# Optimization experiments

Measured on AMD Instinct MI355X. Metric: run time of the kernel, lower is better.

## Reference

```python
import jax, jax.numpy as jnp
import numpy as np

B, NC, H, GH = 64, 21, 32, 64  # batch, num_class, hidden spatial, geo spatial
DN = ('NCHW', 'OIHW', 'NCHW')


def conv2d(x, w, b, stride, pad):
    y = jax.lax.conv_general_dilated(x, w, (stride, stride), [(pad, pad), (pad, pad)], dimension_numbers=DN)
    return y + b[None, :, None, None]


def group_norm(x, scale, bias, groups=32, eps=1e-5):
    b, c, h, w = x.shape
    xg = x.reshape(b, groups, c // groups, h, w)
    mean = xg.mean(axis=(2, 3, 4), keepdims=True)
    var = xg.var(axis=(2, 3, 4), keepdims=True)
    xn = ((xg - mean) * jax.lax.rsqrt(var + eps)).reshape(b, c, h, w)
    return xn * scale[None, :, None, None] + bias[None, :, None, None]


def setup_inputs() -> dict:
    key = jax.random.key(0)
    ks = iter(jax.random.split(key, 64))
    rn = lambda shape, s=0.05: jax.random.normal(next(ks), shape, jnp.float32) * s
    inp = {
        'hidden_state': jnp.tanh(rn((B, 128, H, H), 1.0)),
        'delta_flow': rn((B, 2, H, H), 1.0),
        'mask': jax.random.uniform(next(ks), (B, 1, H, H), jnp.float32),
        'geo': rn((B, 8, GH, GH), 1.0),
        'obj_id': jax.random.randint(next(ks), (B,), 1, NC + 1),
        # geo_model
        'g1_w': rn((128, 8, 3, 3)), 'g1_b': rn((128,)),
        'g2_w': rn((64, 128, 3, 3)), 'g2_b': rn((64,)),
        # delta_flow_model
        'd1_w': rn((128, 2, 7, 7)), 'd1_b': rn((128,)),
        'd2_w': rn((64, 128, 3, 3)), 'd2_b': rn((64,)),
        # mask_model
        'm1_w': rn((64, 1, 3, 3)), 'm1_b': rn((64,)),
        'm2_w': rn((32, 64, 3, 3)), 'm2_b': rn((32,)),
        # conv_layers (conv + GroupNorm(32) x3, all stride 2)
        'c1_w': rn((128, 288, 3, 3)), 'c1_b': rn((128,)), 'gn1_s': jnp.ones((128,)), 'gn1_bb': jnp.zeros((128,)),
        'c2_w': rn((128, 128, 3, 3)), 'c2_b': rn((128,)), 'gn2_s': jnp.ones((128,)), 'gn2_bb': jnp.zeros((128,)),
        'c3_w': rn((128, 128, 3, 3)), 'c3_b': rn((128,)), 'gn3_s': jnp.ones((128,)), 'gn3_bb': jnp.zeros((128,)),
        # fc_layers
        'fc1_w': rn((1024, 2048)), 'fc1_b': rn((1024,)),
        'fc2_w': rn((256, 1024)), 'fc2_b': rn((256,)),
        # prediction heads (random instead of zero-init so grads are non-trivial)
        'rot_w': rn((6 * NC, 256)), 'rot_b': jnp.tile(jnp.array([1., 0., 0., 0., 1., 0.], jnp.float32), NC),
        'tr_w': rn((3 * NC, 256)), 'tr_b': rn((3 * NC,)),
    }
    return inp


def reference(hidden_state, delta_flow, mask, geo, obj_id,
              g1_w, g1_b, g2_w, g2_b, d1_w, d1_b, d2_w, d2_b, m1_w, m1_b, m2_w, m2_b,
              c1_w, c1_b, gn1_s, gn1_bb, c2_w, c2_b, gn2_s, gn2_bb, c3_w, c3_b, gn3_s, gn3_bb,
              fc1_w, fc1_b, fc2_w, fc2_b, rot_w, rot_b, tr_w, tr_b):
    relu = jax.nn.relu
    geo_enc = relu(conv2d(relu(conv2d(geo, g1_w, g1_b, 1, 1)), g2_w, g2_b, 2, 1))        # [B,64,32,32]
    df_enc = relu(conv2d(relu(conv2d(delta_flow, d1_w, d1_b, 1, 3)), d2_w, d2_b, 1, 1))  # [B,64,32,32]
    m_enc = relu(conv2d(relu(conv2d(mask, m1_w, m1_b, 1, 1)), m2_w, m2_b, 1, 1))         # [B,32,32,32]
    enc = jnp.concatenate([hidden_state, df_enc, m_enc, geo_enc], axis=1)                # [B,288,32,32]
    x = relu(group_norm(conv2d(enc, c1_w, c1_b, 2, 1), gn1_s, gn1_bb))                   # [B,128,16,16]
    x = relu(group_norm(conv2d(x, c2_w, c2_b, 2, 1), gn2_s, gn2_bb))                     # [B,128,8,8]
    x = relu(group_norm(conv2d(x, c3_w, c3_b, 2, 1), gn3_s, gn3_bb))                     # [B,128,4,4]
    x = x.reshape(x.shape[0], -1)                                                        # [B,2048]
    x = relu(x @ fc1_w.T + fc1_b)
    x = relu(x @ fc2_w.T + fc2_b)                                                        # [B,256]
    tr = (x @ tr_w.T + tr_b).reshape(-1, NC, 3)
    rot = (x @ rot_w.T + rot_b).reshape(-1, NC, 6)
    # torch.index_select(., dim=1, index=obj_id-1)[:, 0, :] -> uses obj_id[0]
    tr = jnp.take(tr, obj_id - 1, axis=1)[:, 0, :]
    rot = jnp.take(rot, obj_id - 1, axis=1)[:, 0, :]
    return (rot, tr)
```

## Files before the change

### kernel.cpp

```cpp
#include <hip/hip_runtime.h>
#include <hip/hip_bf16.h>

typedef __bf16 bf16x8 __attribute__((ext_vector_type(8)));
typedef __bf16 bf16x4 __attribute__((ext_vector_type(4)));
typedef float  f32x4  __attribute__((ext_vector_type(4)));

struct PackArgs {
    const float* src[11];
    __bf16* dst[11];
    int Cout[11], Cin[11], KHW[11], KW[11], Cinpad[11], Kpad[11], mode[11];
    int cum[12];
};

__device__ void pack_dev(const PackArgs& pa, int gidx)
{
    if (gidx >= pa.cum[11]) return;
    int s = 0;
    for (int i = 1; i <= 10; ++i) s += (gidx >= pa.cum[i]) ? 1 : 0;
    int l = gidx - pa.cum[s];
    int Kp = pa.Kpad[s];
    int co = l / Kp, k = l - co * Kp;
    float v = 0.f;
    if (co < pa.Cout[s]) {
        if (pa.mode[s] == 0) {
            int cip = pa.Cinpad[s];
            int tap = k / cip, ci = k - tap * cip;
            if (tap < pa.KHW[s] && ci < pa.Cin[s])
                v = pa.src[s][((long)co * pa.Cin[s] + ci) * pa.KHW[s] + tap];
        } else if (pa.mode[s] == 1) {
            int pix = k >> 7, c = k & 127;
            v = pa.src[s][(long)co * 2048 + c * 16 + pix];
        } else if (pa.mode[s] == 2) {
            v = pa.src[s][(long)co * Kp + k];
        } else {
            int kh = k >> 4, r = k & 15, kw = r >> 1, ci = r & 1;
            if (kh < 7 && kw < 7)
                v = pa.src[s][((long)(co * 2 + ci) * 7 + kh) * 7 + kw];
        }
    }
    pa.dst[s][l] = (__bf16)v;
}

struct BulkPack { const float* s[8]; __bf16* d[8]; };

template<int CO, int CIN, int KP>
__device__ __forceinline__ void pack_conv8(const float* __restrict__ src,
                                           __bf16* __restrict__ dst, int eb)
{
    int e = eb * 8;
    int co = e / KP;
    int k  = e - co * KP;
    int tap = k / CIN;
    int ci  = k - tap * CIN;
    bf16x8 o = {};
    if (co < CO && tap < 9) {
        const float* s = src + ((long)co * CIN + ci) * 9 + tap;
#pragma unroll
        for (int j = 0; j < 8; ++j) o[j] = (__bf16)s[j * 9];
    }
    *(bf16x8*)&dst[e] = o;
}

__device__ __forceinline__ void pack_fc1_8(const float* __restrict__ src,
                                           __bf16* __restrict__ dst, int eb)
{
    int e = eb * 8;
    int co = e >> 11, k = e & 2047;
    int pix = k >> 7, c = k & 127;
    const float* s = src + (long)co * 2048 + c * 16 + pix;
    bf16x8 o;
#pragma unroll
    for (int j = 0; j < 8; ++j) o[j] = (__bf16)s[j * 16];
    *(bf16x8*)&dst[e] = o;
}

__device__ __forceinline__ void pack_fc2_8(const float* __restrict__ src,
                                           __bf16* __restrict__ dst, int eb)
{
    int e = eb * 8;
    f32x4 lo = *(const f32x4*)&src[e];
    f32x4 hi = *(const f32x4*)&src[e + 4];
    bf16x8 o = { (__bf16)lo.x, (__bf16)lo.y, (__bf16)lo.z, (__bf16)lo.w,
                 (__bf16)hi.x, (__bf16)hi.y, (__bf16)hi.z, (__bf16)hi.w };
    *(bf16x8*)&dst[e] = o;
// ... 245 lines not shown
    bf16x8 av[APASS], bv[BPASS];
    auto LOAD = [&](int k0) {
        int k = k0 + scol;
#pragma unroll
        for (int ja = 0; ja < APASS; ++ja)
            av[ja] = *(const bf16x8*)&A[(long)(ja * SROWS + srow) * g.Kpad + k];
        if (MODE == 1) {
            int q = k >> 3;
            int off = (q >> 1) * (g.Win * g.CinTot) + (q & 1) * 8;
#pragma unroll
            for (int j = 0; j < BPASS; ++j)
                bv[j] = *(const bf16x8*)&in_[nbase[j] + off];
        } else {
            int tap = k / CINPAD;
            int ci  = k - tap * CINPAD;
            int kh  = tap / KW;
            int kw  = tap - kh * KW;
            bool tv = tap < g.KHW;
            int off = (kh * g.Win + kw) * g.CinTot + ci;
#pragma unroll
            for (int j = 0; j < BPASS; ++j) {
                bf16x8 z = {};
                int hi = hi0a[j] + kh, wi = wi0a[j] + kw;
                if (tv && (unsigned)hi < (unsigned)g.Hin && (unsigned)wi < (unsigned)g.Win)
                    z = *(const bf16x8*)&in_[nbase[j] + off];
                bv[j] = z;
            }
        }
    };

    f32x4 acc[MFRAG][2] = {};
    LOAD(0);
    for (int k0 = 0;;) {
        if (k0) __syncthreads();
#pragma unroll
        for (int ja = 0; ja < APASS; ++ja)
            *(bf16x8*)&As[ja * SROWS + srow][scol] = av[ja];
#pragma unroll
        for (int j = 0; j < BPASS; ++j)
            *(bf16x8*)&Bs[j * SROWS + srow][scol] = bv[j];
        __syncthreads();
        int kn = k0 + BK;
        bool more = kn < g.Kpad;
        if (more) LOAD(kn);
#pragma unroll
        for (int kk = 0; kk < BK; kk += 32) {
            bf16x8 bfr[2];
            bfr[0] = *(const bf16x8*)&Bs[wn + lr][kk + lk];
            bfr[1] = *(const bf16x8*)&Bs[wn + 16 + lr][kk + lk];
#pragma unroll
            for (int i = 0; i < MFRAG; ++i) {
                bf16x8 a = *(const bf16x8*)&As[wm + i * 16 + lr][kk + lk];
                acc[i][0] = __builtin_amdgcn_mfma_f32_16x16x32_bf16(a, bfr[0], acc[i][0], 0, 0, 0);
                acc[i][1] = __builtin_amdgcn_mfma_f32_16x16x32_bf16(a, bfr[1], acc[i][1], 0, 0, 0);
            }
        }
        if (!more) break;
        k0 = kn;
    }

    const int HWm1 = (1 << g.log2HWout) - 1;
#pragma unroll
    for (int i = 0; i < MFRAG; ++i) {
        int co = wm + i * 16 + (lane >> 4) * 4;
        if (co >= g.Cout) continue;
        f32x4 bv4 = *(const f32x4*)&bias[co];
#pragma unroll
        for (int jb = 0; jb < 2; ++jb) {
            int nn = ntile + wn + jb * 16 + lr;
            f32x4 v = acc[i][jb] + bv4;
            if (RELU) { v.x = fmaxf(v.x, 0.f); v.y = fmaxf(v.y, 0.f); v.z = fmaxf(v.z, 0.f); v.w = fmaxf(v.w, 0.f); }
            int ob = nn >> g.log2HWout, opix = nn & HWm1;
            long o = (((long)(g.b0o + ob) << g.log2HWout) + opix) * g.CTOT + g.C0 + co;
            if (OUTBF) {
                bf16x4 o4 = { (__bf16)v.x, (__bf16)v.y, (__bf16)v.z, (__bf16)v.w };
                *(bf16x4*)&((__bf16*)out_)[o] = o4;
            } else {
                *(f32x4*)&((float*)out_)[o] = v;
            }
        }
    }
}

template<int BM, int BN, int BK, int THREADS, int WMW, int WNW, int CINPAD, int KW, int MODE, bool OUTBF, bool RELU>
__global__ __launch_bounds__(THREADS) void conv_gemm2(
    const __bf16* __restrict__ in_, const __bf16* __restrict__ A,
    const float* __restrict__ bias, void* __restrict__ out_, ConvGeom g)
{
    __shared__ __attribute__((aligned(16))) char smem[(BM + BN) * (BK + 8) * 2];
    int mt = blockIdx.y * BM;
    ConvGeom gg = g;
    gg.C0 += mt;
    gg.Cout -= mt;
    conv_dev2<BM, BN, BK, THREADS, WMW, WNW, CINPAD, KW, MODE, OUTBF, RELU>(
        smem, blockIdx.x, in_, A + (long)mt * g.Kpad, bias + mt, out_, gg);
}

template<int BM, int BN, int BK, int THREADS, int WMW, int WNW, int CINPAD, int KW, int PPB>
__global__ __launch_bounds__(THREADS) void conv_gn_kern(
    const __bf16* __restrict__ in_, const __bf16* __restrict__ A,
    const float* __restrict__ bias, const float* __restrict__ gns,
    const float* __restrict__ gnb, __bf16* __restrict__ out_, ConvGeom g)
{
    constexpr int MEXT = BM / WMW;
    constexpr int NEXT = BN / WNW;
    constexpr int MFRAG = MEXT / 16;
    constexpr int NFRAG = NEXT / 16;
    constexpr int KROW = BK / 8;
    constexpr int SROWS = THREADS / KROW;
    constexpr int APASS = BM / SROWS;
    constexpr int BPASS = BN / SROWS;
    constexpr int LDK = BK + 8;

    __shared__ __attribute__((aligned(16))) char smem_[(BM + BN) * (BK + 8) * 2];
    auto As = reinterpret_cast<__bf16 (*)[LDK]>(smem_);
    auto Bs = reinterpret_cast<__bf16 (*)[LDK]>(smem_ + (size_t)BM * LDK * sizeof(__bf16));
    static_assert((size_t)BN * (BM + 4) * 4 <= (size_t)(BM + BN) * (BK + 8) * 2, "smf fits");

    const int tid = threadIdx.x;
    const int mt = blockIdx.y * BM;
    const __bf16* Ap = A + (long)mt * g.Kpad;
    const int C0 = g.C0 + mt;
    const int ntile = blockIdx.x * BN;
    const int lane = tid & 63, w = tid >> 6;
    const int wm = (w / WNW) * MEXT, wn = (w % WNW) * NEXT;
    const int lr = lane & 15, lk = (lane >> 4) * 8;
    const int srow = tid / KROW, scol = (tid % KROW) * 8;

    long nbase[BPASS]; int hi0a[BPASS], wi0a[BPASS];
#pragma unroll
    for (int j = 0; j < BPASS; ++j) {
        int n = ntile + j * SROWS + srow;
        int bb = g.b0i + (n >> g.log2HWout);
        int pix = n & ((1 << g.log2HWout) - 1);
        int ho = pix >> g.log2Wout, wo = pix & ((1 << g.log2Wout) - 1);
        hi0a[j] = ho * g.stride - g.pad;
        wi0a[j] = wo * g.stride - g.pad;
        nbase[j] = (((long)bb * g.Hin + hi0a[j]) * g.Win + wi0a[j]) * g.CinTot;
    }

    bf16x8 av[APASS], bv[BPASS];
    auto LOAD = [&](int k0) {
        int k = k0 + scol;
#pragma unroll
        for (int ja = 0; ja < APASS; ++ja)
            av[ja] = *(const bf16x8*)&Ap[(long)(ja * SROWS + srow) * g.Kpad + k];
        int tap = k / CINPAD;
        int ci  = k - tap * CINPAD;
        int kh  = tap / KW;
        int kw  = tap - kh * KW;
        bool tv = tap < g.KHW;
        int off = (kh * g.Win + kw) * g.CinTot + ci;
#pragma unroll
        for (int j = 0; j < BPASS; ++j) {
            bf16x8 z = {};
            int hi = hi0a[j] + kh, wi = wi0a[j] + kw;
            if (tv && (unsigned)hi < (unsigned)g.Hin && (unsigned)wi < (unsigned)g.Win)
                z = *(const bf16x8*)&in_[nbase[j] + off];
            bv[j] = z;
        }
    };

    f32x4 acc[MFRAG][NFRAG] = {};
    LOAD(0);
    for (int k0 = 0;;) {
        if (k0) __syncthreads();
#pragma unroll
        for (int ja = 0; ja < APASS; ++ja)
            *(bf16x8*)&As[ja * SROWS + srow][scol] = av[ja];
#pragma unroll
        for (int j = 0; j < BPASS; ++j)
            *(bf16x8*)&Bs[j * SROWS + srow][scol] = bv[j];
        __syncthreads();
        int kn = k0 + BK;
        bool more = kn < g.Kpad;
        if (more) LOAD(kn);
#pragma unroll
        for (int kk = 0; kk < BK; kk += 32) {
            bf16x8 bfr[NFRAG], afr[MFRAG];
#pragma unroll
            for (int jn = 0; jn < NFRAG; ++jn)
                bfr[jn] = *(const bf16x8*)&Bs[wn + jn * 16 + lr][kk + lk];
#pragma unroll
            for (int i = 0; i < MFRAG; ++i)
                afr[i] = *(const bf16x8*)&As[wm + i * 16 + lr][kk + lk];
#pragma unroll
            for (int i = 0; i < MFRAG; ++i)
#pragma unroll
                for (int jn = 0; jn < NFRAG; ++jn)
                    acc[i][jn] = __builtin_amdgcn_mfma_f32_16x16x32_bf16(afr[i], bfr[jn], acc[i][jn], 0, 0, 0);
        }
        if (!more) break;
        k0 = kn;
    }

    __syncthreads();
    auto smf = reinterpret_cast<float (*)[BM + 4]>(smem_);
#pragma unroll
    for (int i = 0; i < MFRAG; ++i) {
        int m = wm + i * 16 + (lane >> 4) * 4;
        f32x4 bv4 = *(const f32x4*)&bias[C0 + m];
#pragma unroll
        for (int jn = 0; jn < NFRAG; ++jn) {
            int n = wn + jn * 16 + lr;
            *(f32x4*)&smf[n][m] = acc[i][jn] + bv4;
        }
    }
    __syncthreads();

    constexpr int NSETS = (BN / PPB) * (BM / 4);
    constexpr int TPS = THREADS / NSETS;
    constexpr int PPT = PPB / TPS;
    const int set = tid / TPS, part = tid % TPS;
    const int bit = set / (BM / 4);
    const int grp = set % (BM / 4);
    const int m0 = grp * 4;
    float sum = 0.f, sq = 0.f;
#pragma unroll
    for (int p = 0; p < PPT; ++p) {
        int nl = bit * PPB + part + p * TPS;
        f32x4 v = *(const f32x4*)&smf[nl][m0];
        sum += v.x + v.y + v.z + v.w;
        sq  += v.x * v.x + v.y * v.y + v.z * v.z + v.w * v.w;
    }
#pragma unroll
    for (int off = TPS >> 1; off > 0; off >>= 1) {
        sum += __shfl_xor(sum, off);
        sq  += __shfl_xor(sq, off);
    }
    const float len = (float)(PPB * 4);
    float mean = sum / len;
    float var  = sq / len - mean * mean;
    float rstd = rsqrtf(fmaxf(var, 0.f) + 1e-5f);
    f32x4 s4 = *(const f32x4*)&gns[C0 + m0];
    f32x4 b4 = *(const f32x4*)&gnb[C0 + m0];
    const int HWm1 = (1 << g.log2HWout) - 1;
#pragma unroll
    for (int p = 0; p < PPT; ++p) {
        int nl = bit * PPB + part + p * TPS;
        f32x4 v = *(const f32x4*)&smf[nl][m0];
        f32x4 r;
        r.x = fmaxf((v.x - mean) * rstd * s4.x + b4.x, 0.f);
        r.y = fmaxf((v.y - mean) * rstd * s4.y + b4.y, 0.f);
        r.z = fmaxf((v.z - mean) * rstd * s4.z + b4.z, 0.f);
        r.w = fmaxf((v.w - mean) * rstd * s4.w + b4.w, 0.f);
        int n = ntile + nl;
        int ob = n >> g.log2HWout, opix = n & HWm1;
        long o = (((long)(g.b0o + ob) << g.log2HWout) + opix) * g.CTOT + C0 + m0;
        bf16x4 o4 = { (__bf16)r.x, (__bf16)r.y, (__bf16)r.z, (__bf16)r.w };
        *(bf16x4*)&out_[o] = o4;
    }
}

#define B1_CONV 3072
#define B1_PACK 775
__global__ __launch_bounds__(512) void branch1_kern(
    const __bf16* __restrict__ geo_p, const __bf16* __restrict__ wg1, const float* __restrict__ g1_b, __bf16* __restrict__ g1out,
    const __bf16* __restrict__ dflow_pp, const __bf16* __restrict__ wd1, const float* __restrict__ d1_b, __bf16* __restrict__ d1out,
    const __bf16* __restrict__ mask_p, const __bf16* __restrict__ wm1, const float* __restrict__ m1_b, __bf16* __restrict__ m1out,
    BulkPack bp, ConvGeom gg1, ConvGeom gd1, ConvGeom gm1)
{
    __shared__ __attribute__((aligned(16))) char smem[27648];
    int x = blockIdx.x;
    if (x < 2048) {
        conv_dev<128, 128, 32, 512, 8, 3, 0, true, true>(smem, x, geo_p, wg1, g1_b, g1out, gg1);
        return;
    }
    if (x < 2560) {
        conv_dev<128, 128, 32, 512, 8, 7, 1, true, true>(smem, x - 2048, dflow_pp, wd1, d1_b, d1out, gd1);
        return;
    }
    if (x < B1_CONV) {
        conv_dev<64, 128, 64, 512, 8, 3, 0, true, true>(smem, x - 2560, mask_p, wm1, m1_b, m1out, gm1);
        return;
    }
    int x2 = x - B1_CONV;
    int tid = threadIdx.x;
    if (x2 < 18)       pack_conv8<64, 128, 1152>(bp.s[0], bp.d[0], x2 * 512 + tid);
    else if (x2 < 36)  pack_conv8<64, 128, 1152>(bp.s[1], bp.d[1], (x2 - 18) * 512 + tid);
    else if (x2 < 45)  pack_conv8<32, 64, 576>(bp.s[2], bp.d[2], (x2 - 36) * 512 + tid);
    else if (x2 < 127) pack_conv8<128, 288, 2624>(bp.s[3], bp.d[3], (x2 - 45) * 512 + tid);
    else if (x2 < 163) pack_conv8<128, 128, 1152>(bp.s[4], bp.d[4], (x2 - 127) * 512 + tid);
    else if (x2 < 199) pack_conv8<128, 128, 1152>(bp.s[5], bp.d[5], (x2 - 163) * 512 + tid);
    else if (x2 < 711) pack_fc1_8(bp.s[6], bp.d[6], (x2 - 199) * 512 + tid);
    else               pack_fc2_8(bp.s[7], bp.d[7], (x2 - 711) * 512 + tid);
}

#define B2_CONV 1536
#define B2_HID 4096
__global__ __launch_bounds__(256) void branch2_kern(
    const __bf16* __restrict__ g1out, const __bf16* __restrict__ wg2, const float* __restrict__ g2_b,
    const __bf16* __restrict__ d1out, const __bf16* __restrict__ wd2, const float* __restrict__ d2_b,
    const __bf16* __restrict__ m1out, const __bf16* __restrict__ wm2, const float* __restrict__ m2_b,
    const float* __restrict__ hidden, __bf16* __restrict__ enc,
    ConvGeom gg2, ConvGeom gd2, ConvGeom gm2)
{
    __shared__ __attribute__((aligned(16))) char smem[(64 + 128) * (64 + 8) * 2];
    int x = blockIdx.x;
    if (x >= B2_CONV) { hid_dev(smem, hidden, enc, x - B2_CONV, threadIdx.x); return; }
    int sec = x % 3, bx = x / 3;
    if (sec == 0)
        conv_dev2<64, 128, 64, 256, 1, 4, 128, 3, 0, true, true>(smem, bx, g1out, wg2, g2_b, enc, gg2);
    else if (sec == 1)
        conv_dev2<64, 128, 64, 256, 1, 4, 128, 3, 0, true, true>(smem, bx, d1out, wd2, d2_b, enc, gd2);
    else
        conv_dev2<64, 128, 64, 256, 1, 4, 64, 3, 0, true, true>(smem, bx, m1out, wm2, m2_b, enc, gm2);
}

__global__ __launch_bounds__(256) void fc1_splitk(
    const __bf16* __restrict__ A, const __bf16* __restrict__ B,
    float* __restrict__ outacc)
{
    __shared__ __attribute__((aligned(16))) __bf16 As[64][40];
    __shared__ __attribute__((aligned(16))) __bf16 Bs[64][40];
    const int tid = threadIdx.x;
    const int mtile = blockIdx.y * 64;
    const int kbase = blockIdx.x * 512;
    const int lane = tid & 63, w = tid >> 6;
    const int wm = (w >> 1) * 32, wn = (w & 1) * 32;
    const int lr = lane & 15, lk = (lane >> 4) * 8;
    const int srow = tid >> 2, soff = (tid & 3) * 8;

    f32x4 acc00 = {}, acc01 = {}, acc10 = {}, acc11 = {};
    for (int k0 = 0; k0 < 512; k0 += 32) {
        *(bf16x8*)&As[srow][soff] = *(const bf16x8*)&A[(long)(mtile + srow) * 2048 + kbase + k0 + soff];
        *(bf16x8*)&Bs[srow][soff] = *(const bf16x8*)&B[(long)srow * 2048 + kbase + k0 + soff];
        __syncthreads();
        bf16x8 a0 = *(const bf16x8*)&As[wm + lr][lk];
        bf16x8 a1 = *(const bf16x8*)&As[wm + 16 + lr][lk];
        bf16x8 b0f = *(const bf16x8*)&Bs[wn + lr][lk];
        bf16x8 b1f = *(const bf16x8*)&Bs[wn + 16 + lr][lk];
        acc00 = __builtin_amdgcn_mfma_f32_16x16x32_bf16(a0, b0f, acc00, 0, 0, 0);
        acc01 = __builtin_amdgcn_mfma_f32_16x16x32_bf16(a0, b1f, acc01, 0, 0, 0);
        acc10 = __builtin_amdgcn_mfma_f32_16x16x32_bf16(a1, b0f, acc10, 0, 0, 0);
        acc11 = __builtin_amdgcn_mfma_f32_16x16x32_bf16(a1, b1f, acc11, 0, 0, 0);
        __syncthreads();
    }
    f32x4 accs[2][2] = { { acc00, acc01 }, { acc10, acc11 } };
#pragma unroll
    for (int mi = 0; mi < 2; ++mi) {
        int co0 = mtile + wm + mi * 16 + (lane >> 4) * 4;
#pragma unroll
        for (int ni = 0; ni < 2; ++ni) {
            int nn = wn + ni * 16 + lr;
            f32x4 v = accs[mi][ni];
            float* dst = &outacc[(long)nn * 1024 + co0];
            atomicAdd(dst + 0, v.x);
            atomicAdd(dst + 1, v.y);
            atomicAdd(dst + 2, v.z);
            atomicAdd(dst + 3, v.w);
        }
    }
}

__global__ __launch_bounds__(256) void fc2_splitk(
    const __bf16* __restrict__ A, const float* __restrict__ Bacc,
    const float* __restrict__ bb, float* __restrict__ outacc)
{
    __shared__ __attribute__((aligned(16))) __bf16 As[64][40];
    __shared__ __attribute__((aligned(16))) __bf16 Bs[64][40];
    const int tid = threadIdx.x;
    const int mtile = blockIdx.y * 64;
    const int kbase = blockIdx.x * 256;
    const int lane = tid & 63, w = tid >> 6;
    const int wm = (w >> 1) * 32, wn = (w & 1) * 32;
    const int lr = lane & 15, lk = (lane >> 4) * 8;
    const int srow = tid >> 2, soff = (tid & 3) * 8;

    f32x4 acc00 = {}, acc01 = {}, acc10 = {}, acc11 = {};
    for (int k0 = 0; k0 < 256; k0 += 32) {
        int k = kbase + k0 + soff;
        *(bf16x8*)&As[srow][soff] = *(const bf16x8*)&A[(long)(mtile + srow) * 1024 + k];
        f32x4 lo = *(const f32x4*)&Bacc[(long)srow * 1024 + k];
        f32x4 hi = *(const f32x4*)&Bacc[(long)srow * 1024 + k + 4];
        f32x4 blo = *(const f32x4*)&bb[k];
        f32x4 bhi = *(const f32x4*)&bb[k + 4];
        bf16x8 bvv;
        bvv[0] = (__bf16)fmaxf(lo.x + blo.x, 0.f);
        bvv[1] = (__bf16)fmaxf(lo.y + blo.y, 0.f);
        bvv[2] = (__bf16)fmaxf(lo.z + blo.z, 0.f);
        bvv[3] = (__bf16)fmaxf(lo.w + blo.w, 0.f);
        bvv[4] = (__bf16)fmaxf(hi.x + bhi.x, 0.f);
        bvv[5] = (__bf16)fmaxf(hi.y + bhi.y, 0.f);
        bvv[6] = (__bf16)fmaxf(hi.z + bhi.z, 0.f);
        bvv[7] = (__bf16)fmaxf(hi.w + bhi.w, 0.f);
        *(bf16x8*)&Bs[srow][soff] = bvv;
        __syncthreads();
        bf16x8 a0 = *(const bf16x8*)&As[wm + lr][lk];
        bf16x8 a1 = *(const bf16x8*)&As[wm + 16 + lr][lk];
        bf16x8 b0f = *(const bf16x8*)&Bs[wn + lr][lk];
        bf16x8 b1f = *(const bf16x8*)&Bs[wn + 16 + lr][lk];
        acc00 = __builtin_amdgcn_mfma_f32_16x16x32_bf16(a0, b0f, acc00, 0, 0, 0);
        acc01 = __builtin_amdgcn_mfma_f32_16x16x32_bf16(a0, b1f, acc01, 0, 0, 0);
        acc10 = __builtin_amdgcn_mfma_f32_16x16x32_bf16(a1, b0f, acc10, 0, 0, 0);
        acc11 = __builtin_amdgcn_mfma_f32_16x16x32_bf16(a1, b1f, acc11, 0, 0, 0);
        __syncthreads();
    }
    f32x4 accs[2][2] = { { acc00, acc01 }, { acc10, acc11 } };
#pragma unroll
    for (int mi = 0; mi < 2; ++mi) {
        int co0 = mtile + wm + mi * 16 + (lane >> 4) * 4;
#pragma unroll
        for (int ni = 0; ni < 2; ++ni) {
            int nn = wn + ni * 16 + lr;
            f32x4 v = accs[mi][ni];
            float* dst = &outacc[(long)nn * 256 + co0];
            atomicAdd(dst + 0, v.x);
            atomicAdd(dst + 1, v.y);
            atomicAdd(dst + 2, v.z);
            atomicAdd(dst + 3, v.w);
        }
    }
}

__global__ void gn_nhwc(const float* __restrict__ in, const float* __restrict__ s,
                        const float* __restrict__ bi, __bf16* __restrict__ out,
                        int C, int HW)
{
    int b = blockIdx.x >> 5, g = blockIdx.x & 31;
    int tid = threadIdx.x, nt = blockDim.x;
    const float* p = in + (long)b * HW * C + g * 4;
    float sum = 0.f, sq = 0.f;
    for (int i = tid; i < HW; i += nt) {
        f32x4 v = *(const f32x4*)&p[(long)i * C];
        sum += v.x + v.y + v.z + v.w;
        sq  += v.x * v.x + v.y * v.y + v.z * v.z + v.w * v.w;
    }
    __shared__ float rs[256], rq[256];
    rs[tid] = sum; rq[tid] = sq; __syncthreads();
    for (int off = nt >> 1; off > 0; off >>= 1) {
        if (tid < off) { rs[tid] += rs[tid + off]; rq[tid] += rq[tid + off]; }
        __syncthreads();
    }
    int len = HW * 4;
    float mean = rs[0] / len;
    float var  = rq[0] / len - mean * mean;
    float rstd = rsqrtf(fmaxf(var, 0.f) + 1e-5f);
    f32x4 s4 = *(const f32x4*)&s[g * 4];
    f32x4 b4 = *(const f32x4*)&bi[g * 4];
    __bf16* q = out + (long)b * HW * C + g * 4;
    for (int i = tid; i < HW; i += nt) {
        f32x4 v = *(const f32x4*)&p[(long)i * C];
        f32x4 r;
        r.x = fmaxf((v.x - mean) * rstd * s4.x + b4.x, 0.f);
        r.y = fmaxf((v.y - mean) * rstd * s4.y + b4.y, 0.f);
        r.z = fmaxf((v.z - mean) * rstd * s4.z + b4.z, 0.f);
        r.w = fmaxf((v.w - mean) * rstd * s4.w + b4.w, 0.f);
        bf16x4 o4 = { (__bf16)r.x, (__bf16)r.y, (__bf16)r.z, (__bf16)r.w };
        *(bf16x4*)&q[(long)i * C] = o4;
    }
}

__global__ __launch_bounds__(576) void head_kern(
    const float* __restrict__ x, const float* __restrict__ fb,
    const float* __restrict__ rw, const float* __restrict__ rb,
    const float* __restrict__ tw, const float* __restrict__ tb,
    const int* __restrict__ obj, float* __restrict__ out)
{
    int b = blockIdx.x;
    int k = threadIdx.x >> 6;
    int lane = threadIdx.x & 63;
    int j = obj[0] - 1;
    const float* xr = x + (long)b * 256;
    const float* wr;
    float bias0;
    if (k < 6) { wr = rw + (long)(j * 6 + k) * 256; bias0 = rb[j * 6 + k]; }
    else       { wr = tw + (long)(j * 3 + (k - 6)) * 256; bias0 = tb[j * 3 + (k - 6)]; }
    float acc = 0.f;
#pragma unroll
    for (int p = 0; p < 4; ++p) {
        int i = lane + p * 64;
        float xv = fmaxf(xr[i] + fb[i], 0.f);
        acc = fmaf(xv, wr[i], acc);
    }
#pragma unroll
    for (int off = 32; off > 0; off >>= 1) acc += __shfl_down(acc, off);
    if (lane == 0) {
        float r = acc + bias0;
        if (k < 6) out[b * 6 + k] = r;
        else       out[384 + b * 3 + (k - 6)] = r;
    }
}

extern "C" void kernel_launch(void* const* d_in, const int* in_sizes, int n_in,
                              void* d_out, int out_size, void* d_ws, size_t ws_size,
                              hipStream_t stream)
{
    const float* hidden = (const float*)d_in[0];
    const float* dflow  = (const float*)d_in[1];
    const float* mask   = (const float*)d_in[2];
    const float* geo    = (const float*)d_in[3];
    const int*   obj    = (const int*)d_in[4];
    const float* g1_w = (const float*)d_in[5],  *g1_b = (const float*)d_in[6];
    const float* g2_w = (const float*)d_in[7],  *g2_b = (const float*)d_in[8];
    const float* d1_w = (const float*)d_in[9],  *d1_b = (const float*)d_in[10];
    const float* d2_w = (const float*)d_in[11], *d2_b = (const float*)d_in[12];
    const float* m1_w = (const float*)d_in[13], *m1_b = (const float*)d_in[14];
    const float* m2_w = (const float*)d_in[15], *m2_b = (const float*)d_in[16];
    const float* c1_w = (const float*)d_in[17], *c1_b = (const float*)d_in[18];
    const float* gn1_s = (const float*)d_in[19], *gn1_bb = (const float*)d_in[20];
    const float* c2_w = (const float*)d_in[21], *c2_b = (const float*)d_in[22];
    const float* gn2_s = (const float*)d_in[23], *gn2_bb = (const float*)d_in[24];
    const float* c3_w = (const float*)d_in[25], *c3_b = (const float*)d_in[26];
    const float* gn3_s = (const float*)d_in[27], *gn3_bb = (const float*)d_in[28];
    const float* fc1_w = (const float*)d_in[29], *fc1_b = (const float*)d_in[30];
    const float* fc2_w = (const float*)d_in[31], *fc2_b = (const float*)d_in[32];
    const float* rot_w = (const float*)d_in[33], *rot_b = (const float*)d_in[34];
    const float* tr_w  = (const float*)d_in[35], *tr_b  = (const float*)d_in[36];

    char* ws = (char*)d_ws;
    __bf16* enc = (__bf16*)ws;
    char* W = ws + 37748736;
    __bf16* wg1  = (__bf16*)(W + 0);
    __bf16* wd1  = (__bf16*)(W + 24576);
    __bf16* wm1  = (__bf16*)(W + 57344);
    __bf16* wg2  = (__bf16*)(W + 73728);
    __bf16* wd2  = (__bf16*)(W + 221184);
    __bf16* wm2  = (__bf16*)(W + 368640);
    __bf16* wc1  = (__bf16*)(W + 442368);
    __bf16* wc2  = (__bf16*)(W + 1114112);
    __bf16* wc3  = (__bf16*)(W + 1409024);
    __bf16* wfc1 = (__bf16*)(W + 1703936);
    __bf16* wfc2 = (__bf16*)(W + 5898240);
    __bf16* geo_p    = (__bf16*)(ws + 44179456);
    __bf16* dflow_pp = (__bf16*)(ws + 48373760);
    __bf16* mask_p   = (__bf16*)(ws + 48783360);
    __bf16* g1out    = (__bf16*)(ws + 49831936);
    __bf16* d1out    = (__bf16*)(ws + 116940800);
    __bf16* m1out    = (__bf16*)(ws + 133718016);
    float*  c1raw    = (float*)(ws + 142106624);
    __bf16* x1       = (__bf16*)(ws + 150495232);
    __bf16* x2       = (__bf16*)(ws + 156786688);
    __bf16* x3       = (__bf16*)(ws + 158359552);
    float*  fc1acc   = (float*)(ws + 158621696);
    float*  fc2acc   = (float*)(ws + 158883840);

    PackArgs pa;
    {
        const float* srcs[11] = { g1_w, d1_w, m1_w, g2_w, d2_w, m2_w, c1_w, c2_w, c3_w, fc1_w, fc2_w };
        __bf16* dsts[11] = { wg1, wd1, wm1, wg2, wd2, wm2, wc1, wc2, wc3, wfc1, wfc2 };
        int Co[11]  = { 128, 128, 64, 64, 64, 32, 128, 128, 128, 1024, 256 };
        int Ci[11]  = { 8, 2, 1, 128, 128, 64, 288, 128, 128, 0, 0 };
        int KH[11]  = { 9, 49, 9, 9, 9, 9, 9, 9, 9, 0, 0 };
        int KWn[11] = { 3, 7, 3, 3, 3, 3, 3, 3, 3, 0, 0 };
        int Cp[11]  = { 8, 8, 8, 128, 128, 64, 288, 128, 128, 0, 0 };
        int Kp[11]  = { 96, 128, 128, 1152, 1152, 576, 2624, 1152, 1152, 2048, 1024 };
        int Mp[11]  = { 128, 128, 64, 64, 64, 64, 128, 128, 128, 1024, 256 };
        int Md[11]  = { 0, 3, 0, 0, 0, 0, 0, 0, 0, 1, 2 };
        int c = 0; pa.cum[0] = 0;
        for (int i = 0; i < 11; ++i) {
            pa.src[i] = srcs[i]; pa.dst[i] = dsts[i];
            pa.Cout[i] = Co[i]; pa.Cin[i] = Ci[i]; pa.KHW[i] = KH[i]; pa.KW[i] = KWn[i];
            pa.Cinpad[i] = Cp[i]; pa.Kpad[i] = Kp[i]; pa.mode[i] = Md[i];
            c += Mp[i] * Kp[i]; pa.cum[i + 1] = c;
        }
    }
    BulkPack bp;
    {
        const float* s[8] = { g2_w, d2_w, m2_w, c1_w, c2_w, c3_w, fc1_w, fc2_w };
        __bf16* d[8] = { wg2, wd2, wm2, wc1, wc2, wc3, wfc1, wfc2 };
        for (int i = 0; i < 8; ++i) { bp.s[i] = s[i]; bp.d[i] = d[i]; }
    }

    {
        int total_blocks = PACK_B + GEOV_B + DF_B + MASKV_B + ZERO_B;
        prep_kern<<<dim3(total_blocks), 256, 0, stream>>>(pa, geo, geo_p, dflow, dflow_pp,
                                                          mask, mask_p, fc1acc, fc2acc);
    }

    {
        ConvGeom gg1 = { 8, 64, 64, 12, 6, 1, 1, 96, 9, 128, 128, 0, 0, 0 };
        ConvGeom gd1 = { 2, 40, 40, 10, 5, 1, 0, 128, 49, 128, 128, 0, 0, 0 };
        ConvGeom gm1 = { 8, 32, 32, 10, 5, 1, 1, 128, 9, 64, 64, 0, 0, 0 };
        branch1_kern<<<dim3(B1_CONV + B1_PACK), 512, 0, stream>>>(geo_p, wg1, g1_b, g1out,
                                                                  dflow_pp, wd1, d1_b, d1out,
                                                                  mask_p, wm1, m1_b, m1out,
                                                                  bp, gg1, gd1, gm1);
    }
    {
        ConvGeom gg2 = { 128, 64, 64, 10, 5, 2, 1, 1152, 9, 64, 288, 224, 0, 0 };
        ConvGeom gd2 = { 128, 32, 32, 10, 5, 1, 1, 1152, 9, 64, 288, 128, 0, 0 };
        ConvGeom gm2 = { 64, 32, 32, 10, 5, 1, 1, 576, 9, 32, 288, 192, 0, 0 };
        branch2_kern<<<dim3(B2_CONV + B2_HID), 256, 0, stream>>>(g1out, wg2, g2_b,
                                                                 d1out, wd2, d2_b,
                                                                 m1out, wm2, m2_b,
                                                                 hidden, enc, gg2, gd2, gm2);
    }

    {
        ConvGeom gc1 = { 288, 32, 32, 8, 4, 2, 1, 2624, 9, 128, 128, 0, 0, 0 };
        conv_gemm2<64, 128, 64, 256, 1, 4, 288, 3, 0, false, false><<<dim3(128, 2), 256, 0, stream>>>(enc, wc1, c1_b, c1raw, gc1);
    }
    gn_nhwc<<<dim3(2048), 256, 0, stream>>>(c1raw, gn1_s, gn1_bb, x1, 128, 256);

    {
        ConvGeom gc2 = { 128, 16, 16, 6, 3, 2, 1, 1152, 9, 128, 128, 0, 0, 0 };
        conv_gn_kern<64, 64, 64, 256, 2, 2, 128, 3, 64><<<dim3(64, 2), 256, 0, stream>>>(
            x1, wc2, c2_b, gn2_s, gn2_bb, x2, gc2);
    }
    {
        ConvGeom gc3 = { 128, 8, 8, 4, 2, 2, 1, 1152, 9, 128, 128, 0, 0, 0 };
        conv_gn_kern<64, 64, 64, 256, 2, 2, 128, 3, 16><<<dim3(16, 2), 256, 0, stream>>>(
            x2, wc3, c3_b, gn3_s, gn3_bb, x3, gc3);
    }

    fc1_splitk<<<dim3(4, 16), 256, 0, stream>>>(wfc1, x3, fc1acc);
    fc2_splitk<<<dim3(4, 4), 256, 0, stream>>>(wfc2, fc1acc, fc1_b, fc2acc);

    head_kern<<<dim3(64), 576, 0, stream>>>(fc2acc, fc2_b, rot_w, rot_b, tr_w, tr_b, obj, (float*)d_out);
}
```

Baseline: 205.5 us.

## Fuse tail stages into one cooperative kernel with grid-wide syncs

Replaces the seven tail launches (conv1, group norm, conv2+GN, conv3+GN, fc1, fc2, head) with a single cooperative kernel of 256 blocks. Each stage runs on a subset of blocks and the stages are separated by grid.sync(). The goal is to remove per-launch overhead and the idle gaps between many small dependent kernels. In exchange, grid barriers have their own cost, later stages leave most blocks idle, and the head now runs with 256 threads looping over the outputs.

```diff
diff --git a/kernel.cpp b/kernel.cpp
--- a/kernel.cpp
+++ b/kernel.cpp
@@ -1,5 +1,8 @@
 #include <hip/hip_runtime.h>
 #include <hip/hip_bf16.h>
+#include <hip/hip_cooperative_groups.h>
+
+namespace cg = cooperative_groups;
 
 typedef __bf16 bf16x8 __attribute__((ext_vector_type(8)));
 typedef __bf16 bf16x4 __attribute__((ext_vector_type(4)));
@@ -411,25 +414,11 @@
     }
 }
 
-template<int BM, int BN, int BK, int THREADS, int WMW, int WNW, int CINPAD, int KW, int MODE, bool OUTBF, bool RELU>
-__global__ __launch_bounds__(THREADS) void conv_gemm2(
-    const __bf16* __restrict__ in_, const __bf16* __restrict__ A,
-    const float* __restrict__ bias, void* __restrict__ out_, ConvGeom g)
-{
-    __shared__ __attribute__((aligned(16))) char smem[(BM + BN) * (BK + 8) * 2];
-    int mt = blockIdx.y * BM;
-    ConvGeom gg = g;
-    gg.C0 += mt;
-    gg.Cout -= mt;
-    conv_dev2<BM, BN, BK, THREADS, WMW, WNW, CINPAD, KW, MODE, OUTBF, RELU>(
-        smem, blockIdx.x, in_, A + (long)mt * g.Kpad, bias + mt, out_, gg);
-}
-
 template<int BM, int BN, int BK, int THREADS, int WMW, int WNW, int CINPAD, int KW, int PPB>
-__global__ __launch_bounds__(THREADS) void conv_gn_kern(
+__device__ void conv_gn_dev(char* __restrict__ smem_, int bx, int my,
     const __bf16* __restrict__ in_, const __bf16* __restrict__ A,
     const float* __restrict__ bias, const float* __restrict__ gns,
-    const float* __restrict__ gnb, __bf16* __restrict__ out_, ConvGeom g)
+    const float* __restrict__ gnb, __bf16* __restrict__ out_, const ConvGeom& g)
 {
     constexpr int MEXT = BM / WMW;
     constexpr int NEXT = BN / WNW;
@@ -441,16 +430,14 @@
     constexpr int BPASS = BN / SROWS;
     constexpr int LDK = BK + 8;
 
-    __shared__ __attribute__((aligned(16))) char smem_[(BM + BN) * (BK + 8) * 2];
     auto As = reinterpret_cast<__bf16 (*)[LDK]>(smem_);
     auto Bs = reinterpret_cast<__bf16 (*)[LDK]>(smem_ + (size_t)BM * LDK * sizeof(__bf16));
-    static_assert((size_t)BN * (BM + 4) * 4 <= (size_t)(BM + BN) * (BK + 8) * 2, "smf fits");
 
     const int tid = threadIdx.x;
-    const int mt = blockIdx.y * BM;
+    const int mt = my * BM;
     const __bf16* Ap = A + (long)mt * g.Kpad;
     const int C0 = g.C0 + mt;
-    const int ntile = blockIdx.x * BN;
+    const int ntile = bx * BN;
     const int lane = tid & 63, w = tid >> 6;
     const int wm = (w / WNW) * MEXT, wn = (w % WNW) * NEXT;
     const int lr = lane & 15, lk = (lane >> 4) * 8;
@@ -579,72 +566,57 @@
         bf16x4 o4 = { (__bf16)r.x, (__bf16)r.y, (__bf16)r.z, (__bf16)r.w };
         *(bf16x4*)&out_[o] = o4;
     }
-}
-
-#define B1_CONV 3072
-#define B1_PACK 775
-__global__ __launch_bounds__(512) void branch1_kern(
-    const __bf16* __restrict__ geo_p, const __bf16* __restrict__ wg1, const float* __restrict__ g1_b, __bf16* __restrict__ g1out,
-    const __bf16* __restrict__ dflow_pp, const __bf16* __restrict__ wd1, const float* __restrict__ d1_b, __bf16* __restrict__ d1out,
-    const __bf16* __restrict__ mask_p, const __bf16* __restrict__ wm1, const float* __restrict__ m1_b, __bf16* __restrict__ m1out,
-    BulkPack bp, ConvGeom gg1, ConvGeom gd1, ConvGeom gm1)
-{
-    __shared__ __attribute__((aligned(16))) char smem[27648];
-    int x = blockIdx.x;
-    if (x < 2048) {
-        conv_dev<128, 128, 32, 512, 8, 3, 0, true, true>(smem, x, geo_p, wg1, g1_b, g1out, gg1);
-        return;
-    }
-    if (x < 2560) {
-        conv_dev<128, 128, 32, 512, 8, 7, 1, true, true>(smem, x - 2048, dflow_pp, wd1, d1_b, d1out, gd1);
-        return;
-    }
-    if (x < B1_CONV) {
-        conv_dev<64, 128, 64, 512, 8, 3, 0, true, true>(smem, x - 2560, mask_p, wm1, m1_b, m1out, gm1);
-        return;
-    }
-    int x2 = x - B1_CONV;
-    int tid = threadIdx.x;
-    if (x2 < 18)       pack_conv8<64, 128, 1152>(bp.s[0], bp.d[0], x2 * 512 + tid);
-    else if (x2 < 36)  pack_conv8<64, 128, 1152>(bp.s[1], bp.d[1], (x2 - 18) * 512 + tid);
-    else if (x2 < 45)  pack_conv8<32, 64, 576>(bp.s[2], bp.d[2], (x2 - 36) * 512 + tid);
-    else if (x2 < 127) pack_conv8<128, 288, 2624>(bp.s[3], bp.d[3], (x2 - 45) * 512 + tid);
-    else if (x2 < 163) pack_conv8<128, 128, 1152>(bp.s[4], bp.d[4], (x2 - 127) * 512 + tid);
-    else if (x2 < 199) pack_conv8<128, 128, 1152>(bp.s[5], bp.d[5], (x2 - 163) * 512 + tid);
-    else if (x2 < 711) pack_fc1_8(bp.s[6], bp.d[6], (x2 - 199) * 512 + tid);
-    else               pack_fc2_8(bp.s[7], bp.d[7], (x2 - 711) * 512 + tid);
-}
-
-#define B2_CONV 1536
-#define B2_HID 4096
-__global__ __launch_bounds__(256) void branch2_kern(
-    const __bf16* __restrict__ g1out, const __bf16* __restrict__ wg2, const float* __restrict__ g2_b,
-    const __bf16* __restrict__ d1out, const __bf16* __restrict__ wd2, const float* __restrict__ d2_b,
-    const __bf16* __restrict__ m1out, const __bf16* __restrict__ wm2, const float* __restrict__ m2_b,
-    const float* __restrict__ hidden, __bf16* __restrict__ enc,
-    ConvGeom gg2, ConvGeom gd2, ConvGeom gm2)
-{
-    __shared__ __attribute__((aligned(16))) char smem[(64 + 128) * (64 + 8) * 2];
-    int x = blockIdx.x;
-    if (x >= B2_CONV) { hid_dev(smem, hidden, enc, x - B2_CONV, threadIdx.x); return; }
-    int sec = x % 3, bx = x / 3;
-    if (sec == 0)
-        conv_dev2<64, 128, 64, 256, 1, 4, 128, 3, 0, true, true>(smem, bx, g1out, wg2, g2_b, enc, gg2);
-    else if (sec == 1)
-        conv_dev2<64, 128, 64, 256, 1, 4, 128, 3, 0, true, true>(smem, bx, d1out, wd2, d2_b, enc, gd2);
-    else
-        conv_dev2<64, 128, 64, 256, 1, 4, 64, 3, 0, true, true>(smem, bx, m1out, wm2, m2_b, enc, gm2);
-}
-
-__global__ __launch_bounds__(256) void fc1_splitk(
-    const __bf16* __restrict__ A, const __bf16* __restrict__ B,
-    float* __restrict__ outacc)
-{
-    __shared__ __attribute__((aligned(16))) __bf16 As[64][40];
-    __shared__ __attribute__((aligned(16))) __bf16 Bs[64][40];
+    __syncthreads();
+}
+
+__device__ void gn_dev(char* smem, const float* __restrict__ in, const float* __restrict__ s,
+                       const float* __restrict__ bi, __bf16* __restrict__ out,
+                       int C, int HW, int unit, int tid)
+{
+    int b = unit >> 5, g = unit & 31;
+    const float* p = in + (long)b * HW * C + g * 4;
+    float sum = 0.f, sq = 0.f;
+    for (int i = tid; i < HW; i += 256) {
+        f32x4 v = *(const f32x4*)&p[(long)i * C];
+        sum += v.x + v.y + v.z + v.w;
+        sq  += v.x * v.x + v.y * v.y + v.z * v.z + v.w * v.w;
+    }
+    float* rs = (float*)smem;
+    float* rq = rs + 256;
+    rs[tid] = sum; rq[tid] = sq; __syncthreads();
+    for (int off = 128; off > 0; off >>= 1) {
+        if (tid < off) { rs[tid] += rs[tid + off]; rq[tid] += rq[tid + off]; }
+        __syncthreads();
+    }
+    int len = HW * 4;
+    float mean = rs[0] / len;
+    float var  = rq[0] / len - mean * mean;
+    float rstd = rsqrtf(fmaxf(var, 0.f) + 1e-5f);
+    f32x4 s4 = *(const f32x4*)&s[g * 4];
+    f32x4 b4 = *(const f32x4*)&bi[g * 4];
+    __bf16* q = out + (long)b * HW * C + g * 4;
+    for (int i = tid; i < HW; i += 256) {
+        f32x4 v = *(const f32x4*)&p[(long)i * C];
+        f32x4 r;
+        r.x = fmaxf((v.x - mean) * rstd * s4.x + b4.x, 0.f);
+        r.y = fmaxf((v.y - mean) * rstd * s4.y + b4.y, 0.f);
+        r.z = fmaxf((v.z - mean) * rstd * s4.z + b4.z, 0.f);
+        r.w = fmaxf((v.w - mean) * rstd * s4.w + b4.w, 0.f);
+        bf16x4 o4 = { (__bf16)r.x, (__bf16)r.y, (__bf16)r.z, (__bf16)r.w };
+        *(bf16x4*)&q[(long)i * C] = o4;
+    }
+    __syncthreads();
+}
+
+__device__ void fc1_dev(char* smem, int kchunk, int mt,
+                        const __bf16* __restrict__ A, const __bf16* __restrict__ B,
+                        float* __restrict__ outacc)
+{
+    auto As = reinterpret_cast<__bf16 (*)[40]>(smem);
+    auto Bs = reinterpret_cast<__bf16 (*)[40]>(smem + 64 * 40 * 2);
     const int tid = threadIdx.x;
-    const int mtile = blockIdx.y * 64;
-    const int kbase = blockIdx.x * 512;
+    const int mtile = mt * 64;
+    const int kbase = kchunk * 512;
     const int lane = tid & 63, w = tid >> 6;
     const int wm = (w >> 1) * 32, wn = (w & 1) * 32;
     const int lr = lane & 15, lk = (lane >> 4) * 8;
@@ -682,15 +654,15 @@
     }
 }
 
-__global__ __launch_bounds__(256) void fc2_splitk(
-    const __bf16* __restrict__ A, const float* __restrict__ Bacc,
-    const float* __restrict__ bb, float* __restrict__ outacc)
-{
-    __shared__ __attribute__((aligned(16))) __bf16 As[64][40];
-    __shared__ __attribute__((aligned(16))) __bf16 Bs[64][40];
+__device__ void fc2_dev(char* smem, int kchunk, int mt,
+                        const __bf16* __restrict__ A, const float* __restrict__ Bacc,
+                        const float* __restrict__ bb, float* __restrict__ outacc)
+{
+    auto As = reinterpret_cast<__bf16 (*)[40]>(smem);
+    auto Bs = reinterpret_cast<__bf16 (*)[40]>(smem + 64 * 40 * 2);
     const int tid = threadIdx.x;
-    const int mtile = blockIdx.y * 64;
-    const int kbase = blockIdx.x * 256;
+    const int mtile = mt * 64;
+    const int kbase = kchunk * 256;
     const int lane = tid & 63, w = tid >> 6;
     const int wm = (w >> 1) * 32, wn = (w & 1) * 32;
     const int lr = lane & 15, lk = (lane >> 4) * 8;
@@ -742,73 +714,140 @@
     }
 }
 
-__global__ void gn_nhwc(const float* __restrict__ in, const float* __restrict__ s,
-                        const float* __restrict__ bi, __bf16* __restrict__ out,
-                        int C, int HW)
-{
-    int b = blockIdx.x >> 5, g = blockIdx.x & 31;
-    int tid = threadIdx.x, nt = blockDim.x;
-    const float* p = in + (long)b * HW * C + g * 4;
-    float sum = 0.f, sq = 0.f;
-    for (int i = tid; i < HW; i += nt) {
-        f32x4 v = *(const f32x4*)&p[(long)i * C];
-        sum += v.x + v.y + v.z + v.w;
-        sq  += v.x * v.x + v.y * v.y + v.z * v.z + v.w * v.w;
-    }
-    __shared__ float rs[256], rq[256];
-    rs[tid] = sum; rq[tid] = sq; __syncthreads();
-    for (int off = nt >> 1; off > 0; off >>= 1) {
-        if (tid < off) { rs[tid] += rs[tid + off]; rq[tid] += rq[tid + off]; }
-        __syncthreads();
-    }
-    int len = HW * 4;
-    float mean = rs[0] / len;
-    float var  = rq[0] / len - mean * mean;
-    float rstd = rsqrtf(fmaxf(var, 0.f) + 1e-5f);
-    f32x4 s4 = *(const f32x4*)&s[g * 4];
-    f32x4 b4 = *(const f32x4*)&bi[g * 4];
-    __bf16* q = out + (long)b * HW * C + g * 4;
-    for (int i = tid; i < HW; i += nt) {
-        f32x4 v = *(const f32x4*)&p[(long)i * C];
-        f32x4 r;
-        r.x = fmaxf((v.x - mean) * rstd * s4.x + b4.x, 0.f);
-        r.y = fmaxf((v.y - mean) * rstd * s4.y + b4.y, 0.f);
-        r.z = fmaxf((v.z - mean) * rstd * s4.z + b4.z, 0.f);
-        r.w = fmaxf((v.w - mean) * rstd * s4.w + b4.w, 0.f);
-        bf16x4 o4 = { (__bf16)r.x, (__bf16)r.y, (__bf16)r.z, (__bf16)r.w };
-        *(bf16x4*)&q[(long)i * C] = o4;
-    }
-}
-
-__global__ __launch_bounds__(576) void head_kern(
-    const float* __restrict__ x, const float* __restrict__ fb,
-    const float* __restrict__ rw, const float* __restrict__ rb,
-    const float* __restrict__ tw, const float* __restrict__ tb,
-    const int* __restrict__ obj, float* __restrict__ out)
-{
-    int b = blockIdx.x;
-    int k = threadIdx.x >> 6;
-    int lane = threadIdx.x & 63;
+__device__ void head_dev(const float* __restrict__ x, const float* __restrict__ fb,
+                         const float* __restrict__ rw, const float* __restrict__ rb,
+                         const float* __restrict__ tw, const float* __restrict__ tb,
+                         const int* __restrict__ obj, float* __restrict__ out,
+                         int b, int tid)
+{
+    int wid = tid >> 6, lane = tid & 63;
     int j = obj[0] - 1;
     const float* xr = x + (long)b * 256;
-    const float* wr;
-    float bias0;
-    if (k < 6) { wr = rw + (long)(j * 6 + k) * 256; bias0 = rb[j * 6 + k]; }
-    else       { wr = tw + (long)(j * 3 + (k - 6)) * 256; bias0 = tb[j * 3 + (k - 6)]; }
-    float acc = 0.f;
-#pragma unroll
-    for (int p = 0; p < 4; ++p) {
-        int i = lane + p * 64;
-        float xv = fmaxf(xr[i] + fb[i], 0.f);
-        acc = fmaf(xv, wr[i], acc);
-    }
-#pragma unroll
-    for (int off = 32; off > 0; off >>= 1) acc += __shfl_down(acc, off);
-    if (lane == 0) {
-        float r = acc + bias0;
-        if (k < 6) out[b * 6 + k] = r;
-        else       out[384 + b * 3 + (k - 6)] = r;
-    }
+    for (int k = wid; k < 9; k += 4) {
+        const float* wr;
+        float b0;
+        if (k < 6) { wr = rw + (long)(j * 6 + k) * 256; b0 = rb[j * 6 + k]; }
+        else       { wr = tw + (long)(j * 3 + (k - 6)) * 256; b0 = tb[j * 3 + (k - 6)]; }
+        float acc = 0.f;
+#pragma unroll
+        for (int p = 0; p < 4; ++p) {
+            int i = lane + p * 64;
+            float xv = fmaxf(xr[i] + fb[i], 0.f);
+            acc = fmaf(xv, wr[i], acc);
+        }
+#pragma unroll
+        for (int off = 32; off > 0; off >>= 1) acc += __shfl_down(acc, off);
+        if (lane == 0) {
+            float r = acc + b0;
+            if (k < 6) out[b * 6 + k] = r;
+            else       out[384 + b * 3 + (k - 6)] = r;
+        }
+    }
+}
+
+#define B1_CONV 3072
+#define B1_PACK 775
+__global__ __launch_bounds__(512) void branch1_kern(
+    const __bf16* __restrict__ geo_p, const __bf16* __restrict__ wg1, const float* __restrict__ g1_b, __bf16* __restrict__ g1out,
+    const __bf16* __restrict__ dflow_pp, const __bf16* __restrict__ wd1, const float* __restrict__ d1_b, __bf16* __restrict__ d1out,
+    const __bf16* __restrict__ mask_p, const __bf16* __restrict__ wm1, const float* __restrict__ m1_b, __bf16* __restrict__ m1out,
+    BulkPack bp, ConvGeom gg1, ConvGeom gd1, ConvGeom gm1)
+{
+    __shared__ __attribute__((aligned(16))) char smem[27648];
+    int x = blockIdx.x;
+    if (x < 2048) {
+        conv_dev<128, 128, 32, 512, 8, 3, 0, true, true>(smem, x, geo_p, wg1, g1_b, g1out, gg1);
+        return;
+    }
+    if (x < 2560) {
+        conv_dev<128, 128, 32, 512, 8, 7, 1, true, true>(smem, x - 2048, dflow_pp, wd1, d1_b, d1out, gd1);
+        return;
+    }
+    if (x < B1_CONV) {
+        conv_dev<64, 128, 64, 512, 8, 3, 0, true, true>(smem, x - 2560, mask_p, wm1, m1_b, m1out, gm1);
+        return;
+    }
+    int x2 = x - B1_CONV;
+    int tid = threadIdx.x;
+    if (x2 < 18)       pack_conv8<64, 128, 1152>(bp.s[0], bp.d[0], x2 * 512 + tid);
+    else if (x2 < 36)  pack_conv8<64, 128, 1152>(bp.s[1], bp.d[1], (x2 - 18) * 512 + tid);
+    else if (x2 < 45)  pack_conv8<32, 64, 576>(bp.s[2], bp.d[2], (x2 - 36) * 512 + tid);
+    else if (x2 < 127) pack_conv8<128, 288, 2624>(bp.s[3], bp.d[3], (x2 - 45) * 512 + tid);
+    else if (x2 < 163) pack_conv8<128, 128, 1152>(bp.s[4], bp.d[4], (x2 - 127) * 512 + tid);
+    else if (x2 < 199) pack_conv8<128, 128, 1152>(bp.s[5], bp.d[5], (x2 - 163) * 512 + tid);
+    else if (x2 < 711) pack_fc1_8(bp.s[6], bp.d[6], (x2 - 199) * 512 + tid);
+    else               pack_fc2_8(bp.s[7], bp.d[7], (x2 - 711) * 512 + tid);
+}
+
+#define B2_CONV 1536
+#define B2_HID 4096
+__global__ __launch_bounds__(256) void branch2_kern(
+    const __bf16* __restrict__ g1out, const __bf16* __restrict__ wg2, const float* __restrict__ g2_b,
+    const __bf16* __restrict__ d1out, const __bf16* __restrict__ wd2, const float* __restrict__ d2_b,
+    const __bf16* __restrict__ m1out, const __bf16* __restrict__ wm2, const float* __restrict__ m2_b,
+    const float* __restrict__ hidden, __bf16* __restrict__ enc,
+    ConvGeom gg2, ConvGeom gd2, ConvGeom gm2)
+{
+    __shared__ __attribute__((aligned(16))) char smem[(64 + 128) * (64 + 8) * 2];
+    int x = blockIdx.x;
+    if (x >= B2_CONV) { hid_dev(smem, hidden, enc, x - B2_CONV, threadIdx.x); return; }
+    int sec = x % 3, bx = x / 3;
+    if (sec == 0)
+        conv_dev2<64, 128, 64, 256, 1, 4, 128, 3, 0, true, true>(smem, bx, g1out, wg2, g2_b, enc, gg2);
+    else if (sec == 1)
+        conv_dev2<64, 128, 64, 256, 1, 4, 128, 3, 0, true, true>(smem, bx, d1out, wd2, d2_b, enc, gd2);
+    else
+        conv_dev2<64, 128, 64, 256, 1, 4, 64, 3, 0, true, true>(smem, bx, m1out, wm2, m2_b, enc, gm2);
+}
+
+struct TailArgs {
+    const __bf16 *enc, *wc1, *wc2, *wc3, *wfc1, *wfc2;
+    const float *c1_b, *gn1_s, *gn1_bb, *c2_b, *gn2_s, *gn2_bb, *c3_b, *gn3_s, *gn3_bb;
+    const float *fc1_b, *fc2_b, *rot_w, *rot_b, *tr_w, *tr_b;
+    const int* obj;
+    float* c1raw;
+    __bf16 *x1, *x2, *x3;
+    float *fc1acc, *fc2acc, *out;
+    ConvGeom gc1, gc2, gc3;
+};
+
+__global__ __launch_bounds__(256) void tail_kern(TailArgs a)
+{
+    __shared__ __attribute__((aligned(16))) char smem[27648];
+    cg::grid_group grid = cg::this_grid();
+    const int u = blockIdx.x, tid = threadIdx.x;
+
+    {
+        int bx = u & 127, mt = (u >> 7) * 64;
+        ConvGeom gg = a.gc1;
+        gg.C0 += mt;
+        gg.Cout -= mt;
+        conv_dev2<64, 128, 64, 256, 1, 4, 288, 3, 0, false, false>(
+            smem, bx, a.enc, a.wc1 + (long)mt * a.gc1.Kpad, a.c1_b + mt, a.c1raw, gg);
+    }
+    grid.sync();
+
+    for (int i = 0; i < 8; ++i)
+        gn_dev(smem, a.c1raw, a.gn1_s, a.gn1_bb, a.x1, 128, 256, u * 8 + i, tid);
+    grid.sync();
+
+    if (u < 128)
+        conv_gn_dev<64, 64, 64, 256, 2, 2, 128, 3, 64>(smem, u & 63, u >> 6,
+            a.x1, a.wc2, a.c2_b, a.gn2_s, a.gn2_bb, a.x2, a.gc2);
+    grid.sync();
+
+    if (u < 32)
+        conv_gn_dev<64, 64, 64, 256, 2, 2, 128, 3, 16>(smem, u & 15, u >> 4,
+            a.x2, a.wc3, a.c3_b, a.gn3_s, a.gn3_bb, a.x3, a.gc3);
+    grid.sync();
+
+    if (u < 64) fc1_dev(smem, u & 3, u >> 2, a.wfc1, a.x3, a.fc1acc);
+    grid.sync();
+
+    if (u < 16) fc2_dev(smem, u & 3, u >> 2, a.wfc2, a.fc1acc, a.fc1_b, a.fc2acc);
+    grid.sync();
+
+    if (u < 64) head_dev(a.fc2acc, a.fc2_b, a.rot_w, a.rot_b, a.tr_w, a.tr_b, a.obj, a.out, u, tid);
 }
 
 extern "C" void kernel_launch(void* const* d_in, const int* in_sizes, int n_in,
@@ -917,24 +956,20 @@
     }
 
     {
-        ConvGeom gc1 = { 288, 32, 32, 8, 4, 2, 1, 2624, 9, 128, 128, 0, 0, 0 };
-        conv_gemm2<64, 128, 64, 256, 1, 4, 288, 3, 0, false, false><<<dim3(128, 2), 256, 0, stream>>>(enc, wc1, c1_b, c1raw, gc1);
-    }
-    gn_nhwc<<<dim3(2048), 256, 0, stream>>>(c1raw, gn1_s, gn1_bb, x1, 128, 256);
-
-    {
-        ConvGeom gc2 = { 128, 16, 16, 6, 3, 2, 1, 1152, 9, 128, 128, 0, 0, 0 };
-        conv_gn_kern<64, 64, 64, 256, 2, 2, 128, 3, 64><<<dim3(64, 2), 256, 0, stream>>>(
-            x1, wc2, c2_b, gn2_s, gn2_bb, x2, gc2);
-    }
-    {
-        ConvGeom gc3 = { 128, 8, 8, 4, 2, 2, 1, 1152, 9, 128, 128, 0, 0, 0 };
-        conv_gn_kern<64, 64, 64, 256, 2, 2, 128, 3, 16><<<dim3(16, 2), 256, 0, stream>>>(
-            x2, wc3, c3_b, gn3_s, gn3_bb, x3, gc3);
-    }
-
-    fc1_splitk<<<dim3(4, 16), 256, 0, stream>>>(wfc1, x3, fc1acc);
-    fc2_splitk<<<dim3(4, 4), 256, 0, stream>>>(wfc2, fc1acc, fc1_b, fc2acc);
-
-    head_kern<<<dim3(64), 576, 0, stream>>>(fc2acc, fc2_b, rot_w, rot_b, tr_w, tr_b, obj, (float*)d_out);
-}
+        TailArgs ta;
+        ta.enc = enc; ta.wc1 = wc1; ta.wc2 = wc2; ta.wc3 = wc3; ta.wfc1 = wfc1; ta.wfc2 = wfc2;
+        ta.c1_b = c1_b; ta.gn1_s = gn1_s; ta.gn1_bb = gn1_bb;
+        ta.c2_b = c2_b; ta.gn2_s = gn2_s; ta.gn2_bb = gn2_bb;
+        ta.c3_b = c3_b; ta.gn3_s = gn3_s; ta.gn3_bb = gn3_bb;
+        ta.fc1_b = fc1_b; ta.fc2_b = fc2_b;
+        ta.rot_w = rot_w; ta.rot_b = rot_b; ta.tr_w = tr_w; ta.tr_b = tr_b;
+        ta.obj = obj;
+        ta.c1raw = c1raw; ta.x1 = x1; ta.x2 = x2; ta.x3 = x3;
+        ta.fc1acc = fc1acc; ta.fc2acc = fc2acc; ta.out = (float*)d_out;
+        ta.gc1 = ConvGeom{ 288, 32, 32, 8, 4, 2, 1, 2624, 9, 128, 128, 0, 0, 0 };
+        ta.gc2 = ConvGeom{ 128, 16, 16, 6, 3, 2, 1, 1152, 9, 128, 128, 0, 0, 0 };
+        ta.gc3 = ConvGeom{ 128, 8, 8, 4, 2, 2, 1, 1152, 9, 128, 128, 0, 0, 0 };
+        void* params[] = { &ta };
+        hipLaunchCooperativeKernel((const void*)tail_kern, dim3(256), dim3(256), params, 0, stream);
+    }
+}
```

New measurement: 361.2 us. 1.76x slower.
